# Performance work log

Hardware: AMD Instinct MI355X
Metric: run time of the kernel (lower is better)

The kernel has to match this reference:

```python
import jax, jax.numpy as jnp
import numpy as np

STAGE = 100
EPS = 1e-5


def bin_affine(w, shift_aff, sign_aff):
    """Vectorized equivalent of the 100-iteration range-mask loop.
    Original: for i in range(stage): mask = (w >= lo_i) & (w < hi_i);
              shift += w.detach()*shift_aff[i]*mask; sign += w.detach()*sign_aff[i]*mask.
    Equivalent to bucketize + gather + scale. Element equal to w.max() falls
    outside every half-open bin (strict <), so it gets zero, matching torch.
    w is detached in the original, so gradients flow only to the affines.
    """
    wf = w.reshape(-1)
    wmin, wmax = wf.min(), wf.max()
    t = (wf - wmin) / (wmax - wmin) * STAGE
    idx = jnp.floor(t).astype(jnp.int32)
    valid = (idx >= 0) & (idx < STAGE)
    idxc = jnp.clip(idx, 0, STAGE - 1)
    wd = jax.lax.stop_gradient(wf)
    shift = jnp.where(valid, wd * shift_aff[idxc], 0.0)
    sign = jnp.where(valid, wd * sign_aff[idxc], 0.0)
    return shift.reshape(w.shape), sign.reshape(w.shape)


def eff_weight(w, shift_aff, sign_aff):
    # Conv2dShift forward with externally-assigned continuous shift/sign:
    # effective weight = sign * 2**shift (deepshift-style, unrounded).
    shift, sign = bin_affine(w, shift_aff, sign_aff)
    return sign * jnp.exp2(shift)


def conv2d(x, w, stride=1, pad=0, groups=1):
    return jax.lax.conv_general_dilated(
        x, w, (stride, stride), [(pad, pad), (pad, pad)],
        dimension_numbers=("NCHW", "OIHW", "NCHW"), feature_group_count=groups)


def batchnorm(x, g, b):
    m = x.mean((0, 2, 3), keepdims=True)
    v = x.var((0, 2, 3), keepdims=True)
    return (x - m) * jax.lax.rsqrt(v + EPS) * g[None, :, None, None] + b[None, :, None, None]


def setup_inputs() -> dict:
    key = jax.random.key(0)
    ks = jax.random.split(key, 16)
    d = {
        "x": jax.random.normal(ks[0], (32, 256, 56, 56), jnp.float32),
        "w_ds": 0.05 * jax.random.normal(ks[1], (512, 256, 1, 1), jnp.float32),
        "w_c1": 0.05 * jax.random.normal(ks[2], (128, 256, 1, 1), jnp.float32),
        "w_peg": 0.05 * jax.random.normal(ks[3], (128, 1, 3, 3), jnp.float32),
        "w_c2": 0.05 * jax.random.normal(ks[4], (128, 128, 3, 3), jnp.float32),
        "w_c3": 0.05 * jax.random.normal(ks[5], (512, 128, 1, 1), jnp.float32),
        "aff_ds_shift": jax.random.normal(ks[6], (STAGE,), jnp.float32),
        "aff_ds_sign": jax.random.normal(ks[7], (STAGE,), jnp.float32),
        "aff_c1_shift": jax.random.normal(ks[8], (STAGE,), jnp.float32),
        "aff_c1_sign": jax.random.normal(ks[9], (STAGE,), jnp.float32),
        "aff_c2_shift": jax.random.normal(ks[10], (STAGE,), jnp.float32),
        "aff_c2_sign": jax.random.normal(ks[11], (STAGE,), jnp.float32),
        "aff_c3_shift": jax.random.normal(ks[12], (STAGE,), jnp.float32),
        "aff_c3_sign": jax.random.normal(ks[13], (STAGE,), jnp.float32),
        "g_bn_ds": jnp.ones((512,), jnp.float32),
        "b_bn_ds": jnp.zeros((512,), jnp.float32),
        "g_bn1": jnp.ones((128,), jnp.float32),
        "b_bn1": jnp.zeros((128,), jnp.float32),
        "g_bn2": jnp.ones((128,), jnp.float32),
        "b_bn2": jnp.zeros((128,), jnp.float32),
        "g_bn3": jnp.ones((512,), jnp.float32),
        "b_bn3": jnp.zeros((512,), jnp.float32),
    }
    return d


def reference(x, w_ds, w_c1, w_peg, w_c2, w_c3,
              aff_ds_shift, aff_ds_sign, aff_c1_shift, aff_c1_sign,
              aff_c2_shift, aff_c2_sign, aff_c3_shift, aff_c3_sign,
              g_bn_ds, b_bn_ds, g_bn1, b_bn1, g_bn2, b_bn2, g_bn3, b_bn3):
    # main branch (fmap_size == self.fmap_size): bin downsample + conv1/2/3 weights
    wds_e = eff_weight(w_ds, aff_ds_shift, aff_ds_sign)
    wc1_e = eff_weight(w_c1, aff_c1_shift, aff_c1_sign)
    wc2_e = eff_weight(w_c2, aff_c2_shift, aff_c2_sign)
    wc3_e = eff_weight(w_c3, aff_c3_shift, aff_c3_sign)

    # downsample = Conv1x1 -> BN -> ReLU
    residual = jax.nn.relu(batchnorm(conv2d(x, wds_e), g_bn_ds, b_bn_ds))

    h = conv2d(x, wc1_e)                                   # 1x1, 256->128
    h = conv2d(h, w_peg, stride=1, pad=1, groups=128)      # PEG depthwise 3x3
    h = jax.nn.relu(batchnorm(h, g_bn1, b_bn1))            # bn1 + act1
    h = conv2d(h, wc2_e, stride=1, pad=1)                  # 3x3, 128->128
    h = jax.nn.relu(batchnorm(h, g_bn2, b_bn2))            # bn2 + act2
    h = conv2d(h, wc3_e)                                   # 1x1, 128->512
    h = batchnorm(h, g_bn3, b_bn3)                         # bn3
    return jax.nn.relu(h + residual)                       # act3
```

## Files before the change

kernel.cpp:

```cpp
#include <hip/hip_runtime.h>
#include <stdint.h>


#define HW    3136
#define WID   56
#define NB    32
#define FLIP_TENSOR 1

#define OFF_MM    0
#define OFF_SC1   8
#define OFF_BI1   136
#define OFF_SC2   264
#define OFF_BI2   392
#define OFF_SC3   520
#define OFF_BI3   1032
#define OFF_SCDS  1544
#define OFF_BIDS  2056
#define WB_BASE_BYTES 16384ULL
#define WB_M  0ULL
#define WB_C2 163840ULL
#define WB_C3 311296ULL
#define PS1S_B  786432ULL
#define PS1Q_B  802816ULL
#define PS2S_B  819200ULL
#define PS2Q_B  1622016ULL
#define PS3S_B  2424832ULL
#define PS3Q_B  5636096ULL
#define PSDS_B  8847360ULL
#define PSDQ_B  12058624ULL
#define AC_BASE_BYTES 16777216ULL
#define AC_A 0ULL
#define AC_B 12845056ULL
#define AC_C 25690112ULL
#define AC_R 77070336ULL
#define AC_XT AC_C
#define NSLOT 1568

typedef __attribute__((ext_vector_type(8))) short bfrag8;
typedef __attribute__((ext_vector_type(4))) float facc4;

__device__ __forceinline__ unsigned short f2bf(float f) {
  unsigned u = __float_as_uint(f);
  u = u + 0x7FFFu + ((u >> 16) & 1u);
  return (unsigned short)(u >> 16);
}
__device__ __forceinline__ float bf2f(unsigned short h) {
  return __uint_as_float(((unsigned)h) << 16);
}
__device__ __forceinline__ unsigned fmap(float f) {
  unsigned u = __float_as_uint(f);
  return (u & 0x80000000u) ? ~u : (u | 0x80000000u);
}
__device__ __forceinline__ float funmap(unsigned m) {
  unsigned u = (m & 0x80000000u) ? (m & 0x7FFFFFFFu) : ~m;
  return __uint_as_float(u);
}

__device__ __forceinline__ void gload_lds16(const void* g, void* l) {
  __builtin_amdgcn_global_load_lds(
      (const __attribute__((address_space(1))) unsigned int*)g,
      (__attribute__((address_space(3))) unsigned int*)l,
      16, 0, 0);
}

__global__ void k_mm_init(unsigned* mm) {
  int t = threadIdx.x;
  if (t < 4) { mm[2 * t] = 0xFFFFFFFFu; mm[2 * t + 1] = 0u; }
}

__device__ __forceinline__ void tensor_of(int g0, int& tensor, int& local0) {
  if (g0 < 131072)      { tensor = 0; local0 = g0; }
  else if (g0 < 163840) { tensor = 1; local0 = g0 - 131072; }
  else if (g0 < 311296) { tensor = 2; local0 = g0 - 163840; }
  else                  { tensor = 3; local0 = g0 - 311296; }
}

__global__ __launch_bounds__(256) void k_minmax(
    const float* __restrict__ w_ds, const float* __restrict__ w_c1,
    const float* __restrict__ w_c2, const float* __restrict__ w_c3,
    unsigned* __restrict__ mm) {
  __shared__ unsigned smin[256], smax[256];
  int t = threadIdx.x;
  int tensor, local0;
  tensor_of(blockIdx.x * 1024, tensor, local0);
  const float* src = (tensor == 0) ? w_ds : (tensor == 1) ? w_c1 : (tensor == 2) ? w_c2 : w_c3;
  float4 v = *(const float4*)(src + local0 + t * 4);
  unsigned mn, mx;
  {
    unsigned m0 = fmap(v.x), m1 = fmap(v.y), m2 = fmap(v.z), m3 = fmap(v.w);
    mn = min(min(m0, m1), min(m2, m3));
    mx = max(max(m0, m1), max(m2, m3));
  }
  smin[t] = mn; smax[t] = mx;
  __syncthreads();
  for (int s = 128; s > 0; s >>= 1) {
    if (t < s) { smin[t] = min(smin[t], smin[t + s]); smax[t] = max(smax[t], smax[t + s]); }
    __syncthreads();
  }
  if (t == 0) {
    atomicMin(&mm[2 * tensor], smin[0]);
    atomicMax(&mm[2 * tensor + 1], smax[0]);
  }
}

__global__ __launch_bounds__(256) void k_effw(
    const float* __restrict__ w_ds, const float* __restrict__ w_c1,
    const float* __restrict__ w_c2, const float* __restrict__ w_c3,
    const float* __restrict__ sh_ds, const float* __restrict__ sg_ds,
    const float* __restrict__ sh_c1, const float* __restrict__ sg_c1,
    const float* __restrict__ sh_c2, const float* __restrict__ sg_c2,
    const float* __restrict__ sh_c3, const float* __restrict__ sg_c3,
    const unsigned* __restrict__ mm, unsigned short* __restrict__ wb) {
  int t = threadIdx.x;
  int tensor, local0;
  tensor_of(blockIdx.x * 1024, tensor, local0);
  const float* src = (tensor == 0) ? w_ds : (tensor == 1) ? w_c1 : (tensor == 2) ? w_c2 : w_c3;
  const float* sha = (tensor == 0) ? sh_ds : (tensor == 1) ? sh_c1 : (tensor == 2) ? sh_c2 : sh_c3;
  const float* sga = (tensor == 0) ? sg_ds : (tensor == 1) ? sg_c1 : (tensor == 2) ? sg_c2 : sg_c3;
  float wmin = funmap(mm[2 * tensor]);
  float wmax = funmap(mm[2 * tensor + 1]);
  float rng = __fsub_rn(wmax, wmin);
  float I32 = __fdiv_rn(rng, 100.0f);
  float edge100 = __fadd_rn(wmin, __fmul_rn(100.0f, I32));
  bool s32 = (wmax < edge100);
  bool binmax = (tensor == FLIP_TENSOR) ? !s32 : s32;
  float4 v4 = *(const float4*)(src + local0 + t * 4);
  float vs[4] = {v4.x, v4.y, v4.z, v4.w};
#pragma unroll
  for (int e = 0; e < 4; ++e) {
    int l = local0 + t * 4 + e;
    float v = vs[e];
    float ew;
    if (v == wmax) {
      ew = binmax ? (v * sga[99]) * exp2f(v * sha[99]) : 0.0f;
    } else {
      float tt = __fmul_rn(__fdiv_rn(__fsub_rn(v, wmin), rng), 100.0f);
      int idx = (int)floorf(tt);
      bool valid = (idx >= 0) && (idx < 100);
      int ic = valid ? idx : 0;
      float shift = valid ? v * sha[ic] : 0.0f;
      float sign  = valid ? v * sga[ic] : 0.0f;
      ew = sign * exp2f(shift);
    }
    unsigned short h = f2bf(ew);
    if (tensor == 0) {
      int co = l >> 8, ci = l & 255;
      wb[WB_M + (size_t)(128 + co) * 256 + ci] = h;
    } else if (tensor == 1) {
      int co = l >> 8, ci = l & 255;
      wb[WB_M + (size_t)co * 256 + ci] = h;
    } else if (tensor == 2) {
      int co = l / 1152; int r2 = l - co * 1152;
      int ci = r2 / 9; int tap = r2 - ci * 9;
      wb[WB_C2 + (size_t)co * 1152 + tap * 128 + ci] = h;
    } else {
      int co = l >> 7, ci = l & 127;
      wb[WB_C3 + (size_t)co * 128 + ci] = h;
    }
  }
}

__global__ __launch_bounds__(256) void k_tr(
    const float* __restrict__ x, unsigned short* __restrict__ XT) {
  __shared__ short lt[64 * 258];
  int bid = blockIdx.x;
  int sp_blk = bid % 49, n = bid / 49;
  int s0 = sp_blk * 64;
  int t = threadIdx.x;
  {
    const float* row = x + ((size_t)n * 256 + t) * HW + s0;
#pragma unroll
    for (int i = 0; i < 16; ++i) {
      float4 v = *(const float4*)(row + i * 4);
      lt[(i * 4 + 0) * 258 + t] = (short)f2bf(v.x);
      lt[(i * 4 + 1) * 258 + t] = (short)f2bf(v.y);
      lt[(i * 4 + 2) * 258 + t] = (short)f2bf(v.z);
      lt[(i * 4 + 3) * 258 + t] = (short)f2bf(v.w);
    }
  }
  __syncthreads();
  {
    int spi = t >> 2, cb = (t & 3) * 64;
    unsigned short* dst = XT + ((size_t)n * HW + s0 + spi) * 256 + cb;
    const short* srcl = &lt[spi * 258 + cb];
#pragma unroll
    for (int q = 0; q < 8; ++q)
      *(float4*)((short*)dst + q * 8) = *(const float4*)(srcl + q * 8);
  }
}

__global__ __launch_bounds__(256) void k_applyT(
    const unsigned short* __restrict__ A, const float* __restrict__ sc,
    const float* __restrict__ bi, unsigned short* __restrict__ A2) {
  __shared__ short lt[64 * 130];
  int bid = blockIdx.x;
  int sp_blk = bid % 49, n = bid / 49;
  int s0 = sp_blk * 64;
  int t = threadIdx.x;
  {
    int c = t >> 1, part = (t & 1) * 32;
    float s = sc[c], b = bi[c];
    const unsigned short* src = A + ((size_t)n * 128 + c) * HW + s0 + part;
#pragma unroll
    for (int q = 0; q < 4; ++q) {
      float4 raw = *(const float4*)(src + q * 8);
      const unsigned short* pv = (const unsigned short*)&raw;
#pragma unroll
      for (int jj = 0; jj < 8; ++jj) {
        float f = fmaxf(fmaf(bf2f(pv[jj]), s, b), 0.0f);
        lt[(part + q * 8 + jj) * 130 + c] = (short)f2bf(f);
      }
    }
  }
  __syncthreads();
  {
    int spi = t >> 2, cb = (t & 3) * 32;
    unsigned short* dst = A2 + ((size_t)n * HW + s0 + spi) * 128 + cb;
    const short* srcl = &lt[spi * 130 + cb];
#pragma unroll
    for (int q = 0; q < 4; ++q)
      *(float4*)((short*)dst + q * 8) = *(const float4*)(srcl + q * 8);
  }
}

__global__ __launch_bounds__(256) void k_mconvG(
    const unsigned short* __restrict__ XT, const unsigned short* __restrict__ Wt,
    unsigned short* __restrict__ Y1, unsigned short* __restrict__ Y2,
    float* __restrict__ PS, float* __restrict__ PQ) {
  __shared__ short lx[64 * 128];
  __shared__ float redS[128][2], redQ[128][2];
  const int tid  = threadIdx.x;
  const int lane = tid & 63;
  const int wv   = tid >> 6;
  int lid = blockIdx.x;
  int xcd = lid & 7;
  int j   = lid >> 3;
  int co_blk = j % 5;
  int t_  = xcd * 196 + j / 5;
  int sp_blk = t_ % 49;
  int n      = t_ / 49;
  const int s0  = sp_blk * 64;
  const int co0 = co_blk * 128;
  const size_t nsp0 = (size_t)n * HW + s0;

  const int wco  = (wv >> 1) * 64;
  const int wsp  = (wv & 1) * 32;
  const int lrow = lane & 15;
  const int lkg  = lane >> 4;
  const int kb8  = lkg * 8;

  int spl[2];
#pragma unroll
  for (int nn = 0; nn < 2; ++nn) spl[nn] = wsp + nn * 16 + lrow;

  facc4 acc[4][2];
#pragma unroll
  for (int m = 0; m < 4; ++m)
#pragma unroll
    for (int nn = 0; nn < 2; ++nn) acc[m][nn] = (facc4)(0.0f);

#pragma unroll
  for (int ph = 0; ph < 2; ++ph) {
    const int k0 = ph * 128;
    __syncthreads();
#pragma unroll
    for (int i = 0; i < 4; ++i) {
      int B  = tid * 16 + i * 4096;
      int sp = B >> 8;
      int p  = (B >> 4) & 15;
      int c  = p ^ (sp & 7);
      const unsigned short* g = XT + (nsp0 + sp) * 256 + k0 + c * 8;
      gload_lds16(g, (char*)lx + B);
    }
    __syncthreads();
    bfrag8 af[4][4];
#pragma unroll
    for (int kk = 0; kk < 4; ++kk)
#pragma unroll
      for (int m = 0; m < 4; ++m)
        af[kk][m] = *(const bfrag8*)(Wt +
            (size_t)(co0 + wco + m * 16 + lrow) * 256 + k0 + kk * 32 + kb8);
#pragma unroll
    for (int kk = 0; kk < 4; ++kk) {
#pragma unroll
      for (int nn = 0; nn < 2; ++nn) {
        int row = spl[nn];
        int chunk = (kk * 4 + lkg) ^ (row & 7);
        bfrag8 b = *(const bfrag8*)((const char*)lx + row * 256 + (chunk << 4));
#pragma unroll
        for (int m = 0; m < 4; ++m)
          acc[m][nn] = __builtin_amdgcn_mfma_f32_16x16x32_bf16(
              af[kk][m], b, acc[m][nn], 0, 0, 0);
      }
    }
  }
  {
    unsigned short* Yb;
    int coL, COst;
    if (co0 < 128) { Yb = Y1; coL = co0; COst = 128; }
    else           { Yb = Y2; coL = co0 - 128; COst = 512; }
#pragma unroll
    for (int m = 0; m < 4; ++m)
#pragma unroll
      for (int nn = 0; nn < 2; ++nn)
#pragma unroll
        for (int r = 0; r < 4; ++r) {
          int co_g = coL + wco + m * 16 + lkg * 4 + r;
          int sp_g = s0 + wsp + nn * 16 + lrow;
          Yb[((size_t)n * COst + co_g) * HW + sp_g] = f2bf(acc[m][nn][r]);
        }
  }
  if (co0 >= 128) {
#pragma unroll
    for (int m = 0; m < 4; ++m)
#pragma unroll
      for (int r = 0; r < 4; ++r) {
        float sv = acc[m][0][r] + acc[m][1][r];
        float qv = acc[m][0][r] * acc[m][0][r] + acc[m][1][r] * acc[m][1][r];
#pragma unroll
        for (int d = 1; d < 16; d <<= 1) {
          sv += __shfl_xor(sv, d);
          qv += __shfl_xor(qv, d);
        }
        if (lrow == 0) {
          int col = wco + m * 16 + lkg * 4 + r;
          redS[col][wv & 1] = sv;
          redQ[col][wv & 1] = qv;
        }
      }
    __syncthreads();
    if (tid < 128) {
      int cstat = co0 - 128 + tid;
      int slot = n * 49 + sp_blk;
      PS[(size_t)cstat * NSLOT + slot] = redS[tid][0] + redS[tid][1];
      PQ[(size_t)cstat * NSLOT + slot] = redQ[tid][0] + redQ[tid][1];
    }
  }
}

__global__ __launch_bounds__(256) void k_mconvG3(
    const unsigned short* __restrict__ A2, const unsigned short* __restrict__ Wt,
    unsigned short* __restrict__ Y,
    float* __restrict__ PS, float* __restrict__ PQ) {
  __shared__ short lx[64 * 128];
  __shared__ float redS[128][2], redQ[128][2];
  const int tid  = threadIdx.x;
  const int lane = tid & 63;
  const int wv   = tid >> 6;
  int lid = blockIdx.x;
  int xcd = lid & 7;
  int j   = lid >> 3;
  int co_blk = j % 4;
  int t_  = xcd * 196 + j / 4;
  int sp_blk = t_ % 49;
  int n      = t_ / 49;
  const int s0  = sp_blk * 64;
  const int co0 = co_blk * 128;
  const size_t nsp0 = (size_t)n * HW + s0;

  const int wco  = (wv >> 1) * 64;
  const int wsp  = (wv & 1) * 32;
  const int lrow = lane & 15;
  const int lkg  = lane >> 4;
  const int kb8  = lkg * 8;

  int spl[2];
#pragma unroll
  for (int nn = 0; nn < 2; ++nn) spl[nn] = wsp + nn * 16 + lrow;

  facc4 acc[4][2];
#pragma unroll
  for (int m = 0; m < 4; ++m)
#pragma unroll
    for (int nn = 0; nn < 2; ++nn) acc[m][nn] = (facc4)(0.0f);

#pragma unroll
  for (int i = 0; i < 4; ++i) {
    int B  = tid * 16 + i * 4096;
    int sp = B >> 8;
    int p  = (B >> 4) & 15;
    int c  = p ^ (sp & 7);
    const unsigned short* g = A2 + (nsp0 + sp) * 128 + c * 8;
    gload_lds16(g, (char*)lx + B);
  }
  __syncthreads();
  bfrag8 af[4][4];
#pragma unroll
  for (int kk = 0; kk < 4; ++kk)
#pragma unroll
    for (int m = 0; m < 4; ++m)
      af[kk][m] = *(const bfrag8*)(Wt +
          (size_t)(co0 + wco + m * 16 + lrow) * 128 + kk * 32 + kb8);
#pragma unroll
  for (int kk = 0; kk < 4; ++kk) {
#pragma unroll
    for (int nn = 0; nn < 2; ++nn) {
      int row = spl[nn];
      int chunk = (kk * 4 + lkg) ^ (row & 7);
      bfrag8 b = *(const bfrag8*)((const char*)lx + row * 256 + (chunk << 4));
#pragma unroll
      for (int m = 0; m < 4; ++m)
        acc[m][nn] = __builtin_amdgcn_mfma_f32_16x16x32_bf16(
            af[kk][m], b, acc[m][nn], 0, 0, 0);
    }
  }
#pragma unroll
  for (int m = 0; m < 4; ++m)
#pragma unroll
    for (int nn = 0; nn < 2; ++nn)
#pragma unroll
      for (int r = 0; r < 4; ++r) {
        int co_g = co0 + wco + m * 16 + lkg * 4 + r;
        int sp_g = s0 + wsp + nn * 16 + lrow;
        Y[((size_t)n * 512 + co_g) * HW + sp_g] = f2bf(acc[m][nn][r]);
      }
  {
#pragma unroll
    for (int m = 0; m < 4; ++m)
#pragma unroll
      for (int r = 0; r < 4; ++r) {
        float sv = acc[m][0][r] + acc[m][1][r];
        float qv = acc[m][0][r] * acc[m][0][r] + acc[m][1][r] * acc[m][1][r];
#pragma unroll
        for (int d = 1; d < 16; d <<= 1) {
          sv += __shfl_xor(sv, d);
          qv += __shfl_xor(qv, d);
        }
        if (lrow == 0) {
          int col = wco + m * 16 + lkg * 4 + r;
          redS[col][wv & 1] = sv;
          redQ[col][wv & 1] = qv;
        }
      }
    __syncthreads();
    if (tid < 128) {
      int cstat = co0 + tid;
      int slot = n * 49 + sp_blk;
      PS[(size_t)cstat * NSLOT + slot] = redS[tid][0] + redS[tid][1];
      PQ[(size_t)cstat * NSLOT + slot] = redQ[tid][0] + redQ[tid][1];
    }
  }
}

template <int CI, int TAPS, int KBLK, int COOUT, bool XBF,
          bool FUSEIN, bool STATS, int NCOB>
__global__ __launch_bounds__(256) void k_mconv6(
    const void* __restrict__ Xv, const unsigned short* __restrict__ Wt,
    unsigned short* __restrict__ Y1,
    const float* __restrict__ fsc, const float* __restrict__ fbi,
    float* __restrict__ PS, float* __restrict__ PQ) {
  constexpr int NSP = (TAPS == 9) ? 192 : 64;
  constexpr int ST  = KBLK + 2;
  __shared__ short lx[NSP][ST];
  __shared__ float redS[128][2], redQ[128][2];
  const int tid  = threadIdx.x;
  const int lane = tid & 63;
  const int wv   = tid >> 6;
  int lid = blockIdx.x;
  int xcd = lid & 7;
  int j   = lid >> 3;
  int co_blk = j % NCOB;
  int t_  = xcd * 196 + j / NCOB;
  int sp_blk = t_ % 49;
  int n      = t_ / 49;
  const int s0  = sp_blk * 64;
  const int co0 = co_blk * 128;
  const int NK  = CI * TAPS;
  const unsigned short* Xh = (const unsigned short*)Xv + (size_t)n * CI * HW;

  const int wco  = (wv >> 1) * 64;
  const int wsp  = (wv & 1) * 32;
  const int lrow = lane & 15;
  const int lkg  = lane >> 4;
  const int kb8  = lkg * 8;

  int spl[2], yc[2], xc[2];
#pragma unroll
  for (int nn = 0; nn < 2; ++nn) {
    spl[nn] = wsp + nn * 16 + lrow;
    int s = s0 + spl[nn];
    yc[nn] = s / WID;
    xc[nn] = s - yc[nn] * WID;
  }

  facc4 acc[4][2];
#pragma unroll
  for (int m = 0; m < 4; ++m)
#pragma unroll
    for (int nn = 0; nn < 2; ++nn) acc[m][nn] = (facc4)(0.0f);

  for (int k0 = 0; k0 < CI; k0 += KBLK) {
    __syncthreads();
    {
#pragma unroll
      for (int i = 0; i < 3; ++i) {
        int task = tid + i * 256;
        int spi = task % 192;
        int kc  = task / 192;
        int p = s0 - 64 + spi;
        short v[8];
        if ((unsigned)p < (unsigned)HW) {
          const unsigned short* pp = Xh + (size_t)(k0 + kc * 8) * HW + p;
#pragma unroll
          for (int jj = 0; jj < 8; ++jj) {
            if (FUSEIN) {
              float f = bf2f(pp[(size_t)jj * HW]);
              f = fmaxf(fmaf(f, fsc[k0 + kc * 8 + jj], fbi[k0 + kc * 8 + jj]), 0.0f);
              v[jj] = (short)f2bf(f);
            } else {
              v[jj] = (short)pp[(size_t)jj * HW];
            }
          }
        } else {
#pragma unroll
          for (int jj = 0; jj < 8; ++jj) v[jj] = 0;
        }
        *(short4*)(&lx[spi][kc * 8])     = (short4){v[0], v[1], v[2], v[3]};
        *(short4*)(&lx[spi][kc * 8 + 4]) = (short4){v[4], v[5], v[6], v[7]};
      }
    }
    __syncthreads();
    {
      bfrag8 afc[4], afn[4];
#pragma unroll
      for (int m = 0; m < 4; ++m)
        afc[m] = *(const bfrag8*)(Wt +
            (size_t)(co0 + wco + m * 16 + lrow) * NK + k0 + kb8);
      for (int tap = 0; tap < 9; ++tap) {
        if (tap < 8) {
#pragma unroll
          for (int m = 0; m < 4; ++m)
            afn[m] = *(const bfrag8*)(Wt +
                (size_t)(co0 + wco + m * 16 + lrow) * NK + (tap + 1) * CI + k0 + kb8);
        }
        const int dy = tap / 3 - 1;
        const int dx = tap % 3 - 1;
        const int off = dy * WID + dx;
#pragma unroll
        for (int nn = 0; nn < 2; ++nn) {
          bfrag8 b = *(const bfrag8*)(&lx[64 + spl[nn] + off][kb8]);
          bool valid = ((unsigned)(xc[nn] + dx) < (unsigned)WID) &&
                       ((unsigned)(yc[nn] + dy) < (unsigned)WID);
          if (!valid) b = (bfrag8)(short)0;
#pragma unroll
          for (int m = 0; m < 4; ++m)
            acc[m][nn] = __builtin_amdgcn_mfma_f32_16x16x32_bf16(
                afc[m], b, acc[m][nn], 0, 0, 0);
        }
#pragma unroll
        for (int m = 0; m < 4; ++m) afc[m] = afn[m];
      }
    }
  }
#pragma unroll
  for (int m = 0; m < 4; ++m)
#pragma unroll
    for (int nn = 0; nn < 2; ++nn)
#pragma unroll
      for (int r = 0; r < 4; ++r) {
        int co_g = co0 + wco + m * 16 + lkg * 4 + r;
        int sp_g = s0 + wsp + nn * 16 + lrow;
        Y1[((size_t)n * COOUT + co_g) * HW + sp_g] = f2bf(acc[m][nn][r]);
      }
  if (STATS) {
#pragma unroll
    for (int m = 0; m < 4; ++m)
#pragma unroll
      for (int r = 0; r < 4; ++r) {
        float sv = acc[m][0][r] + acc[m][1][r];
        float qv = acc[m][0][r] * acc[m][0][r] + acc[m][1][r] * acc[m][1][r];
#pragma unroll
        for (int d = 1; d < 16; d <<= 1) {
          sv += __shfl_xor(sv, d);
          qv += __shfl_xor(qv, d);
        }
        if (lrow == 0) {
          int col = wco + m * 16 + lkg * 4 + r;
          redS[col][wv & 1] = sv;
          redQ[col][wv & 1] = qv;
        }
      }
    __syncthreads();
    if (tid < 128) {
      int cstat = co0 + tid;
      int slot = n * 49 + sp_blk;
      PS[(size_t)cstat * NSLOT + slot] = redS[tid][0] + redS[tid][1];
      PQ[(size_t)cstat * NSLOT + slot] = redQ[tid][0] + redQ[tid][1];
    }
  }
}

__global__ __launch_bounds__(256) void k_dw(
    const unsigned short* __restrict__ Xin, const float* __restrict__ wp,
    unsigned short* __restrict__ Yout,
    float* __restrict__ PS, float* __restrict__ PQ) {
  __shared__ float pl[HW];
  __shared__ float rs[256], rq[256];
  int bid = blockIdx.x;
  int c = bid & 127;
  int n = bid >> 7;
  const unsigned short* src = Xin + (size_t)bid * HW;
  int t = threadIdx.x;
  for (int q = t; q < HW / 4; q += 256) {
    ushort4 h4 = *(const ushort4*)(src + q * 4);
    pl[q * 4 + 0] = bf2f(h4.x); pl[q * 4 + 1] = bf2f(h4.y);
    pl[q * 4 + 2] = bf2f(h4.z); pl[q * 4 + 3] = bf2f(h4.w);
  }
  float w[9];
#pragma unroll
  for (int k = 0; k < 9; ++k) w[k] = wp[c * 9 + k];
  __syncthreads();
  unsigned short* dst = Yout + (size_t)bid * HW;
  float accS = 0.0f, accQ = 0.0f;
  for (int q = t; q < HW / 4; q += 256) {
    float o[4];
#pragma unroll
    for (int e = 0; e < 4; ++e) {
      int s = q * 4 + e;
      int y = s / WID, xcc = s - y * WID;
      float accv = 0.0f;
#pragma unroll
      for (int ky = 0; ky < 3; ++ky) {
        int yy = y + ky - 1;
        if (yy < 0 || yy >= WID) continue;
#pragma unroll
        for (int kx = 0; kx < 3; ++kx) {
          int xx = xcc + kx - 1;
          if (xx < 0 || xx >= WID) continue;
          accv = fmaf(w[ky * 3 + kx], pl[yy * WID + xx], accv);
        }
      }
      o[e] = accv;
      accS += accv;
      accQ = fmaf(accv, accv, accQ);
    }
    ushort4 ov;
    ov.x = f2bf(o[0]); ov.y = f2bf(o[1]); ov.z = f2bf(o[2]); ov.w = f2bf(o[3]);
    *(ushort4*)(dst + q * 4) = ov;
  }
  rs[t] = accS; rq[t] = accQ;
  __syncthreads();
  for (int st = 128; st > 0; st >>= 1) {
    if (t < st) { rs[t] += rs[t + st]; rq[t] += rq[t + st]; }
    __syncthreads();
  }
  if (t == 0) {
    PS[(size_t)c * NB + n] = rs[0];
    PQ[(size_t)c * NB + n] = rq[0];
  }
}

__global__ __launch_bounds__(256) void k_red(
    const float* __restrict__ S, const float* __restrict__ Q,
    const float* __restrict__ g, const float* __restrict__ b,
    float* __restrict__ sc_o, float* __restrict__ bi_o, int npart) {
  int c = blockIdx.x, t = threadIdx.x;
  double s = 0.0, q = 0.0;
  for (int i = t; i < npart; i += 256) {
    s += S[(size_t)c * npart + i];
    q += Q[(size_t)c * npart + i];
  }
  __shared__ double ss[256], qq[256];
  ss[t] = s; qq[t] = q;
  __syncthreads();
  for (int st = 128; st > 0; st >>= 1) {
    if (t < st) { ss[t] += ss[t + st]; qq[t] += qq[t + st]; }
    __syncthreads();
  }
  if (t == 0) {
    double nn = (double)HW * NB;
    double mean = ss[0] / nn;
    double var = qq[0] / nn - mean * mean;
    float rstd = (float)(1.0 / sqrt(var + 1e-5));
    float sc = g[c] * rstd;
    sc_o[c] = sc;
    bi_o[c] = b[c] - (float)mean * sc;
  }
}

__global__ __launch_bounds__(256) void k_final(
    float* __restrict__ out, const unsigned short* __restrict__ hC,
    const unsigned short* __restrict__ r,
    const float* __restrict__ sc3, const float* __restrict__ bi3,
    const float* __restrict__ scds, const float* __restrict__ bids) {
  const int QPN = 512 * 784;
  const int total = NB * QPN;
  for (int q = blockIdx.x * 256 + threadIdx.x; q < total; q += gridDim.x * 256) {
    int qn = q % QPN;
    int c = qn / 784;
    ushort4 hh = *(const ushort4*)(hC + (size_t)q * 4);
    ushort4 rh = *(const ushort4*)(r + (size_t)q * 4);
    float s3 = sc3[c], b3 = bi3[c], sd = scds[c], bd = bids[c];
    float4 o;
    float rb;
    rb = fmaxf(fmaf(bf2f(rh.x), sd, bd), 0.0f); o.x = fmaxf(fmaf(bf2f(hh.x), s3, b3) + rb, 0.0f);
    rb = fmaxf(fmaf(bf2f(rh.y), sd, bd), 0.0f); o.y = fmaxf(fmaf(bf2f(hh.y), s3, b3) + rb, 0.0f);
    rb = fmaxf(fmaf(bf2f(rh.z), sd, bd), 0.0f); o.z = fmaxf(fmaf(bf2f(hh.z), s3, b3) + rb, 0.0f);
    rb = fmaxf(fmaf(bf2f(rh.w), sd, bd), 0.0f); o.w = fmaxf(fmaf(bf2f(hh.w), s3, b3) + rb, 0.0f);
    *(float4*)(out + (size_t)q * 4) = o;
  }
}

extern "C" void kernel_launch(void* const* d_in, const int* in_sizes, int n_in,
                              void* d_out, int out_size, void* d_ws, size_t ws_size,
                              hipStream_t stream) {
  const float *x = nullptr, *w_ds = nullptr, *w_c1 = nullptr, *w_peg = nullptr,
              *w_c2 = nullptr, *w_c3 = nullptr;
  const float* aff[8] = {nullptr};
  const float* v512[4] = {nullptr};
  const float* v128[4] = {nullptr};
  int naff = 0, n512 = 0, n128 = 0;
  for (int i = 0; i < n_in; ++i) {
    const float* p = (const float*)d_in[i];
    switch (in_sizes[i]) {
      case 25690112: x = p; break;
      case 131072:   w_ds = p; break;
      case 32768:    w_c1 = p; break;
      case 1152:     w_peg = p; break;
      case 147456:   w_c2 = p; break;
      case 65536:    w_c3 = p; break;
      case 100:      if (naff < 8) aff[naff++] = p; break;
      case 512:      if (n512 < 4) v512[n512++] = p; break;
      case 128:      if (n128 < 4) v128[n128++] = p; break;
      default: break;
    }
  }
  const float *a_ds_sh = aff[0], *a_ds_sg = aff[1], *a_c1_sh = aff[2], *a_c1_sg = aff[3];
  const float *a_c2_sh = aff[4], *a_c2_sg = aff[5], *a_c3_sh = aff[6], *a_c3_sg = aff[7];
  const float *g_ds = v512[0], *b_ds = v512[1], *g3 = v512[2], *b3 = v512[3];
  const float *g1 = v128[0], *b1 = v128[1], *g2 = v128[2], *b2 = v128[3];

  float* ws  = (float*)d_ws;
  float* out = (float*)d_out;
  unsigned* mm = (unsigned*)(ws + OFF_MM);
  unsigned short* wb = (unsigned short*)((char*)d_ws + WB_BASE_BYTES);
  unsigned short* ac = (unsigned short*)((char*)d_ws + AC_BASE_BYTES);
  unsigned short* bufA  = ac + AC_A;
  unsigned short* bufB  = ac + AC_B;
  unsigned short* bufC  = ac + AC_C;
  unsigned short* bufR  = ac + AC_R;
  unsigned short* bufXT = ac + AC_XT;
  unsigned short* bufA2 = ac + AC_B;
  float* ps1S = (float*)((char*)d_ws + PS1S_B);
  float* ps1Q = (float*)((char*)d_ws + PS1Q_B);
  float* ps2S = (float*)((char*)d_ws + PS2S_B);
  float* ps2Q = (float*)((char*)d_ws + PS2Q_B);
  float* ps3S = (float*)((char*)d_ws + PS3S_B);
  float* ps3Q = (float*)((char*)d_ws + PS3Q_B);
  float* psdS = (float*)((char*)d_ws + PSDS_B);
  float* psdQ = (float*)((char*)d_ws + PSDQ_B);

  k_mm_init<<<dim3(1), dim3(64), 0, stream>>>(mm);
  k_minmax<<<dim3(368), dim3(256), 0, stream>>>(w_ds, w_c1, w_c2, w_c3, mm);
  k_effw<<<dim3(368), dim3(256), 0, stream>>>(
      w_ds, w_c1, w_c2, w_c3,
      a_ds_sh, a_ds_sg, a_c1_sh, a_c1_sg, a_c2_sh, a_c2_sg, a_c3_sh, a_c3_sg,
      mm, wb);
  k_tr<<<dim3(1568), dim3(256), 0, stream>>>(x, bufXT);

  k_mconvG<<<dim3(7840), dim3(256), 0, stream>>>(
      bufXT, wb + WB_M, bufA, bufR, psdS, psdQ);
  k_red<<<dim3(512), dim3(256), 0, stream>>>(psdS, psdQ, g_ds, b_ds,
                                             ws + OFF_SCDS, ws + OFF_BIDS, NSLOT);
  k_dw<<<dim3(NB * 128), dim3(256), 0, stream>>>(bufA, w_peg, bufB, ps1S, ps1Q);
  k_red<<<dim3(128), dim3(256), 0, stream>>>(ps1S, ps1Q, g1, b1,
                                             ws + OFF_SC1, ws + OFF_BI1, NB);
  k_mconv6<128, 9, 32, 128, true, true, true, 1>
      <<<dim3(1568), dim3(256), 0, stream>>>(
      bufB, wb + WB_C2, bufA, ws + OFF_SC1, ws + OFF_BI1, ps2S, ps2Q);
  k_red<<<dim3(128), dim3(256), 0, stream>>>(ps2S, ps2Q, g2, b2,
                                             ws + OFF_SC2, ws + OFF_BI2, NSLOT);
  k_applyT<<<dim3(1568), dim3(256), 0, stream>>>(bufA, ws + OFF_SC2, ws + OFF_BI2,
                                                 bufA2);
  k_mconvG3<<<dim3(6272), dim3(256), 0, stream>>>(
      bufA2, wb + WB_C3, bufC, ps3S, ps3Q);
  k_red<<<dim3(512), dim3(256), 0, stream>>>(ps3S, ps3Q, g3, b3,
                                             ws + OFF_SC3, ws + OFF_BI3, NSLOT);
  k_final<<<dim3(4096), dim3(256), 0, stream>>>(out, bufC, bufR,
                                                ws + OFF_SC3, ws + OFF_BI3,
                                                ws + OFF_SCDS, ws + OFF_BIDS);
}
```

Measured before the change: 552.9 us.

## Replace 3x3 conv kernel with transposed-layout async-LDS MFMA kernel

```diff
diff --git a/kernel.cpp b/kernel.cpp
--- a/kernel.cpp
+++ b/kernel.cpp
@@ -34,6 +34,7 @@
 #define AC_C 25690112ULL
 #define AC_R 77070336ULL
 #define AC_XT AC_C
+#define AC_B2 (AC_C + 25690112ULL)
 #define NSLOT 1568
 
 typedef __attribute__((ext_vector_type(8))) short bfrag8;
@@ -338,6 +339,121 @@
   }
 }
 
+__global__ __launch_bounds__(256) void k_mconvG2(
+    const unsigned short* __restrict__ B2, const unsigned short* __restrict__ Wt,
+    unsigned short* __restrict__ Y,
+    float* __restrict__ PS, float* __restrict__ PQ) {
+  __shared__ short lx[192 * 128];
+  __shared__ float redS[128][2], redQ[128][2];
+  const int tid  = threadIdx.x;
+  const int lane = tid & 63;
+  const int wv   = tid >> 6;
+  int lid = blockIdx.x;
+  int xcd = lid & 7;
+  int j   = lid >> 3;
+  int t_  = xcd * 196 + j;
+  int sp_blk = t_ % 49;
+  int n      = t_ / 49;
+  const int s0 = sp_blk * 64;
+
+  const int wco  = (wv >> 1) * 64;
+  const int wsp  = (wv & 1) * 32;
+  const int lrow = lane & 15;
+  const int lkg  = lane >> 4;
+  const int kb8  = lkg * 8;
+
+  int spl[2], yc[2], xc[2];
+#pragma unroll
+  for (int nn = 0; nn < 2; ++nn) {
+    spl[nn] = wsp + nn * 16 + lrow;
+    int s = s0 + spl[nn];
+    yc[nn] = s / WID;
+    xc[nn] = s - yc[nn] * WID;
+  }
+
+  facc4 acc[4][2];
+#pragma unroll
+  for (int m = 0; m < 4; ++m)
+#pragma unroll
+    for (int nn = 0; nn < 2; ++nn) acc[m][nn] = (facc4)(0.0f);
+
+#pragma unroll
+  for (int i = 0; i < 12; ++i) {
+    int B   = tid * 16 + i * 4096;
+    int row = B >> 8;
+    int p   = (B >> 4) & 15;
+    int c   = p ^ (row & 7);
+    int p0  = s0 - 64 + row;
+    int pc  = (p0 < 0) ? 0 : ((p0 >= HW) ? HW - 1 : p0);
+    const unsigned short* g = B2 + ((size_t)n * HW + pc) * 128 + c * 8;
+    gload_lds16(g, (char*)lx + B);
+  }
+  __syncthreads();
+  for (int tap = 0; tap < 9; ++tap) {
+    const int dy = tap / 3 - 1;
+    const int dx = tap % 3 - 1;
+    const int off = dy * WID + dx;
+    bfrag8 af[4][4];
+#pragma unroll
+    for (int kk = 0; kk < 4; ++kk)
+#pragma unroll
+      for (int m = 0; m < 4; ++m)
+        af[kk][m] = *(const bfrag8*)(Wt +
+            (size_t)(wco + m * 16 + lrow) * 1152 + tap * 128 + kk * 32 + kb8);
+#pragma unroll
+    for (int nn = 0; nn < 2; ++nn) {
+      int row = 64 + spl[nn] + off;
+      bool valid = ((unsigned)(xc[nn] + dx) < (unsigned)WID) &&
+                   ((unsigned)(yc[nn] + dy) < (unsigned)WID);
+#pragma unroll
+      for (int kk = 0; kk < 4; ++kk) {
+        int chunk = (kk * 4 + lkg) ^ (row & 7);
+        bfrag8 b = *(const bfrag8*)((const char*)lx + row * 256 + (chunk << 4));
+        if (!valid) b = (bfrag8)(short)0;
+#pragma unroll
+        for (int m = 0; m < 4; ++m)
+          acc[m][nn] = __builtin_amdgcn_mfma_f32_16x16x32_bf16(
+              af[kk][m], b, acc[m][nn], 0, 0, 0);
+      }
+    }
+  }
+#pragma unroll
+  for (int m = 0; m < 4; ++m)
+#pragma unroll
+    for (int nn = 0; nn < 2; ++nn)
+#pragma unroll
+      for (int r = 0; r < 4; ++r) {
+        int co_g = wco + m * 16 + lkg * 4 + r;
+        int sp_g = s0 + wsp + nn * 16 + lrow;
+        Y[((size_t)n * 128 + co_g) * HW + sp_g] = f2bf(acc[m][nn][r]);
+      }
+  {
+#pragma unroll
+    for (int m = 0; m < 4; ++m)
+#pragma unroll
+      for (int r = 0; r < 4; ++r) {
+        float sv = acc[m][0][r] + acc[m][1][r];
+        float qv = acc[m][0][r] * acc[m][0][r] + acc[m][1][r] * acc[m][1][r];
+#pragma unroll
+        for (int d = 1; d < 16; d <<= 1) {
+          sv += __shfl_xor(sv, d);
+          qv += __shfl_xor(qv, d);
+        }
+        if (lrow == 0) {
+          int col = wco + m * 16 + lkg * 4 + r;
+          redS[col][wv & 1] = sv;
+          redQ[col][wv & 1] = qv;
+        }
+      }
+    __syncthreads();
+    if (tid < 128) {
+      int slot = n * 49 + sp_blk;
+      PS[(size_t)tid * NSLOT + slot] = redS[tid][0] + redS[tid][1];
+      PQ[(size_t)tid * NSLOT + slot] = redQ[tid][0] + redQ[tid][1];
+    }
+  }
+}
+
 __global__ __launch_bounds__(256) void k_mconvG3(
     const unsigned short* __restrict__ A2, const unsigned short* __restrict__ Wt,
     unsigned short* __restrict__ Y,
@@ -415,154 +531,6 @@
         Y[((size_t)n * 512 + co_g) * HW + sp_g] = f2bf(acc[m][nn][r]);
       }
   {
-#pragma unroll
-    for (int m = 0; m < 4; ++m)
-#pragma unroll
-      for (int r = 0; r < 4; ++r) {
-        float sv = acc[m][0][r] + acc[m][1][r];
-        float qv = acc[m][0][r] * acc[m][0][r] + acc[m][1][r] * acc[m][1][r];
-#pragma unroll
-        for (int d = 1; d < 16; d <<= 1) {
-          sv += __shfl_xor(sv, d);
-          qv += __shfl_xor(qv, d);
-        }
-        if (lrow == 0) {
-          int col = wco + m * 16 + lkg * 4 + r;
-          redS[col][wv & 1] = sv;
-          redQ[col][wv & 1] = qv;
-        }
-      }
-    __syncthreads();
-    if (tid < 128) {
-      int cstat = co0 + tid;
-      int slot = n * 49 + sp_blk;
-      PS[(size_t)cstat * NSLOT + slot] = redS[tid][0] + redS[tid][1];
-      PQ[(size_t)cstat * NSLOT + slot] = redQ[tid][0] + redQ[tid][1];
-    }
-  }
-}
-
-template <int CI, int TAPS, int KBLK, int COOUT, bool XBF,
-          bool FUSEIN, bool STATS, int NCOB>
-__global__ __launch_bounds__(256) void k_mconv6(
-    const void* __restrict__ Xv, const unsigned short* __restrict__ Wt,
-    unsigned short* __restrict__ Y1,
-    const float* __restrict__ fsc, const float* __restrict__ fbi,
-    float* __restrict__ PS, float* __restrict__ PQ) {
-  constexpr int NSP = (TAPS == 9) ? 192 : 64;
-  constexpr int ST  = KBLK + 2;
-  __shared__ short lx[NSP][ST];
-  __shared__ float redS[128][2], redQ[128][2];
-  const int tid  = threadIdx.x;
-  const int lane = tid & 63;
-  const int wv   = tid >> 6;
-  int lid = blockIdx.x;
-  int xcd = lid & 7;
-  int j   = lid >> 3;
-  int co_blk = j % NCOB;
-  int t_  = xcd * 196 + j / NCOB;
-  int sp_blk = t_ % 49;
-  int n      = t_ / 49;
-  const int s0  = sp_blk * 64;
-  const int co0 = co_blk * 128;
-  const int NK  = CI * TAPS;
-  const unsigned short* Xh = (const unsigned short*)Xv + (size_t)n * CI * HW;
-
-  const int wco  = (wv >> 1) * 64;
-  const int wsp  = (wv & 1) * 32;
-  const int lrow = lane & 15;
-  const int lkg  = lane >> 4;
-  const int kb8  = lkg * 8;
-
-  int spl[2], yc[2], xc[2];
-#pragma unroll
-  for (int nn = 0; nn < 2; ++nn) {
-    spl[nn] = wsp + nn * 16 + lrow;
-    int s = s0 + spl[nn];
-    yc[nn] = s / WID;
-    xc[nn] = s - yc[nn] * WID;
-  }
-
-  facc4 acc[4][2];
-#pragma unroll
-  for (int m = 0; m < 4; ++m)
-#pragma unroll
-    for (int nn = 0; nn < 2; ++nn) acc[m][nn] = (facc4)(0.0f);
-
-  for (int k0 = 0; k0 < CI; k0 += KBLK) {
-    __syncthreads();
-    {
-#pragma unroll
-      for (int i = 0; i < 3; ++i) {
-        int task = tid + i * 256;
-        int spi = task % 192;
-        int kc  = task / 192;
-        int p = s0 - 64 + spi;
-        short v[8];
-        if ((unsigned)p < (unsigned)HW) {
-          const unsigned short* pp = Xh + (size_t)(k0 + kc * 8) * HW + p;
-#pragma unroll
-          for (int jj = 0; jj < 8; ++jj) {
-            if (FUSEIN) {
-              float f = bf2f(pp[(size_t)jj * HW]);
-              f = fmaxf(fmaf(f, fsc[k0 + kc * 8 + jj], fbi[k0 + kc * 8 + jj]), 0.0f);
-              v[jj] = (short)f2bf(f);
-            } else {
-              v[jj] = (short)pp[(size_t)jj * HW];
-            }
-          }
-        } else {
-#pragma unroll
-          for (int jj = 0; jj < 8; ++jj) v[jj] = 0;
-        }
-        *(short4*)(&lx[spi][kc * 8])     = (short4){v[0], v[1], v[2], v[3]};
-        *(short4*)(&lx[spi][kc * 8 + 4]) = (short4){v[4], v[5], v[6], v[7]};
-      }
-    }
-    __syncthreads();
-    {
-      bfrag8 afc[4], afn[4];
-#pragma unroll
-      for (int m = 0; m < 4; ++m)
-        afc[m] = *(const bfrag8*)(Wt +
-            (size_t)(co0 + wco + m * 16 + lrow) * NK + k0 + kb8);
-      for (int tap = 0; tap < 9; ++tap) {
-        if (tap < 8) {
-#pragma unroll
-          for (int m = 0; m < 4; ++m)
-            afn[m] = *(const bfrag8*)(Wt +
-                (size_t)(co0 + wco + m * 16 + lrow) * NK + (tap + 1) * CI + k0 + kb8);
-        }
-        const int dy = tap / 3 - 1;
-        const int dx = tap % 3 - 1;
-        const int off = dy * WID + dx;
-#pragma unroll
-        for (int nn = 0; nn < 2; ++nn) {
-          bfrag8 b = *(const bfrag8*)(&lx[64 + spl[nn] + off][kb8]);
-          bool valid = ((unsigned)(xc[nn] + dx) < (unsigned)WID) &&
-                       ((unsigned)(yc[nn] + dy) < (unsigned)WID);
-          if (!valid) b = (bfrag8)(short)0;
-#pragma unroll
-          for (int m = 0; m < 4; ++m)
-            acc[m][nn] = __builtin_amdgcn_mfma_f32_16x16x32_bf16(
-                afc[m], b, acc[m][nn], 0, 0, 0);
-        }
-#pragma unroll
-        for (int m = 0; m < 4; ++m) afc[m] = afn[m];
-      }
-    }
-  }
-#pragma unroll
-  for (int m = 0; m < 4; ++m)
-#pragma unroll
-    for (int nn = 0; nn < 2; ++nn)
-#pragma unroll
-      for (int r = 0; r < 4; ++r) {
-        int co_g = co0 + wco + m * 16 + lkg * 4 + r;
-        int sp_g = s0 + wsp + nn * 16 + lrow;
-        Y1[((size_t)n * COOUT + co_g) * HW + sp_g] = f2bf(acc[m][nn][r]);
-      }
-  if (STATS) {
 #pragma unroll
     for (int m = 0; m < 4; ++m)
 #pragma unroll
@@ -740,6 +708,7 @@
   unsigned short* bufC  = ac + AC_C;
   unsigned short* bufR  = ac + AC_R;
   unsigned short* bufXT = ac + AC_XT;
+  unsigned short* bufB2 = ac + AC_B2;
   unsigned short* bufA2 = ac + AC_B;
   float* ps1S = (float*)((char*)d_ws + PS1S_B);
   float* ps1Q = (float*)((char*)d_ws + PS1Q_B);
@@ -765,9 +734,10 @@
   k_dw<<<dim3(NB * 128), dim3(256), 0, stream>>>(bufA, w_peg, bufB, ps1S, ps1Q);
   k_red<<<dim3(128), dim3(256), 0, stream>>>(ps1S, ps1Q, g1, b1,
                                              ws + OFF_SC1, ws + OFF_BI1, NB);
-  k_mconv6<128, 9, 32, 128, true, true, true, 1>
-      <<<dim3(1568), dim3(256), 0, stream>>>(
-      bufB, wb + WB_C2, bufA, ws + OFF_SC1, ws + OFF_BI1, ps2S, ps2Q);
+  k_applyT<<<dim3(1568), dim3(256), 0, stream>>>(bufB, ws + OFF_SC1, ws + OFF_BI1,
+                                                 bufB2);
+  k_mconvG2<<<dim3(1568), dim3(256), 0, stream>>>(
+      bufB2, wb + WB_C2, bufA, ps2S, ps2Q);
   k_red<<<dim3(128), dim3(256), 0, stream>>>(ps2S, ps2Q, g2, b2,
                                              ws + OFF_SC2, ws + OFF_BI2, NSLOT);
   k_applyT<<<dim3(1568), dim3(256), 0, stream>>>(bufA, ws + OFF_SC2, ws + OFF_BI2,
```

New measurement: 552.6 us. No clear change (-0.1%).
